# Kernel tuning notes

Hardware: AMD Instinct MI355X
Metric: run time of the kernel (lower is better)

Reference implementation:

```python
import jax, jax.numpy as jnp
import numpy as np

B, N, K1, M, D = 8, 4096, 17, 2, 256
NT = B * N          # total nodes
EPS = 1e-5          # PyG LayerNorm default eps


def setup_inputs() -> dict:
    key = jax.random.key(0)
    ks = jax.random.split(key, 13)
    s = 1.0 / np.sqrt(D)
    return {
        "x": jax.random.normal(ks[0], (NT, M, D), jnp.float32),
        "knn_edges": jax.random.randint(ks[1], (B, N, K1), 0, N),
        "edge_mask": jax.random.bernoulli(ks[2], 0.9, (B, N, K1)),
        "W0": jax.random.normal(ks[3], (D, D), jnp.float32) * s,
        "b0": jnp.zeros((D,), jnp.float32),
        "g0": jnp.ones((D,), jnp.float32),
        "be0": jnp.zeros((D,), jnp.float32),
        "a0": jnp.full((1,), 0.25, jnp.float32),
        "W1": jax.random.normal(ks[4], (D, D), jnp.float32) * s,
        "b1": jnp.zeros((D,), jnp.float32),
        "g1": jnp.ones((D,), jnp.float32),
        "be1": jnp.zeros((D,), jnp.float32),
        "a1": jnp.full((1,), 0.25, jnp.float32),
    }


def knn_to_edges(knn_edges, edge_mask):
    # drop self column 0, add per-graph batch offsets; keep fixed E with 0/1 weights
    e = knn_edges[:, :, 1:]                       # [B, N, K]
    m = edge_mask[:, :, 1:]
    off = (jnp.arange(B) * N)[:, None, None]      # [B,1,1]
    src = jnp.broadcast_to(jnp.arange(N)[None, :, None] + off, e.shape).reshape(-1)
    dst = (e + off).reshape(-1)
    w = m.reshape(-1).astype(jnp.float32)         # invalid edges -> weight 0
    return src, dst, w


def gcn_conv(h_in, W, b, src, dst, w):
    # PyG GCNConv: add self-loops (weight 1), symmetric normalization
    h = h_in @ W                                            # [NT, D]
    deg = jax.ops.segment_sum(w, dst, num_segments=NT) + 1.0
    dinv = jax.lax.rsqrt(deg)                               # [NT]
    norm = dinv[src] * w * dinv[dst]                        # [E]
    agg = jax.ops.segment_sum(norm[:, None] * h[src], dst, num_segments=NT)
    agg = agg + (dinv * dinv)[:, None] * h                  # self-loop term
    return agg + b


def graph_layernorm(x, g, b):
    # PyG LayerNorm mode='graph', batch=None: normalize over all nodes+features
    xc = x - jnp.mean(x)
    std = jnp.sqrt(jnp.mean(xc * xc))
    return g * (xc / (std + EPS)) + b


def prelu(x, a):
    return jnp.where(x >= 0, x, a * x)


def reference(x, knn_edges, edge_mask, W0, b0, g0, be0, a0, W1, b1, g1, be1, a1):
    src, dst, w = knn_to_edges(knn_edges, edge_mask)
    h = x[:, 0, :]                                          # [NT, D]
    for (W, b, g, be, a) in ((W0, b0, g0, be0, a0), (W1, b1, g1, be1, a1)):
        h = gcn_conv(h, W, b, src, dst, w)
        h = graph_layernorm(h, g, be)
        h = prelu(h, a)
    return h
```

## Files before the change

kernel.cpp:

```cpp
#include <hip/hip_runtime.h>
#include <hip/hip_bf16.h>
#include <stdint.h>

#define B_   8
#define N_   4096
#define K1_  17
#define D_   256
#define NT_  (B_*N_)
#define E16_ (NT_*16)
#define NP_  (NT_*D_)
#define EPS_ 1e-5f

typedef __attribute__((ext_vector_type(8))) short short8v;
typedef __attribute__((ext_vector_type(4))) short short4v;
typedef __attribute__((ext_vector_type(4))) float f32x4;

__device__ __forceinline__ unsigned short f2bfu(float f){
  unsigned u = __float_as_uint(f);
  unsigned r = (u + 0x7FFFu + ((u>>16)&1u)) >> 16;
  return (unsigned short)r;
}
__device__ __forceinline__ short f2bf(float f){ return (short)f2bfu(f); }
__device__ __forceinline__ unsigned pkbf(float lo, float hi){
  return (unsigned)f2bfu(lo) | ((unsigned)f2bfu(hi) << 16);
}
__device__ __forceinline__ float bf2f(short s){
  return __uint_as_float(((unsigned)(unsigned short)s) << 16);
}
__device__ __forceinline__ void unpack2(unsigned u, float& lo, float& hi){
  lo = __uint_as_float(u << 16);
  hi = __uint_as_float(u & 0xFFFF0000u);
}

__global__ __launch_bounds__(256) void k_prep(const float* __restrict__ W0,
                                              const float* __restrict__ W1,
                                              short* __restrict__ Wt0,
                                              short* __restrict__ Wt1,
                                              int* __restrict__ degcnt,
                                              const unsigned int* __restrict__ mw,
                                              int* __restrict__ flag){
  if (blockIdx.x < 128){
    const float* W  = (blockIdx.x & 1) ? W1  : W0;
    short*       Wt = (blockIdx.x & 1) ? Wt1 : Wt0;
    int tile = blockIdx.x >> 1;
    int ti = tile >> 3, tj = tile & 7;
    __shared__ float sm[32][33];
    int r = threadIdx.x >> 5, c = threadIdx.x & 31;
    #pragma unroll
    for (int i=0;i<4;i++)
      sm[r + i*8][c] = W[(ti*32 + r + i*8)*256 + tj*32 + c];
    __syncthreads();
    #pragma unroll
    for (int i=0;i<4;i++){
      int rr = r + i*8;
      Wt[(size_t)(tj*32 + rr)*256 + ti*32 + c] = f2bf(sm[c][rr]);
    }
  } else {
    int ib = blockIdx.x - 128;
    int i  = ib*256 + threadIdx.x;
    degcnt[i] = 0;
    if (ib == 0){
      __shared__ int s_int, s_f32;
      if (threadIdx.x==0){ s_int=1; s_f32=1; }
      __syncthreads();
      int bad_i=0, bad_f=0;
      #pragma unroll
      for (int j=0;j<4;j++){
        unsigned w = mw[threadIdx.x*4 + j];
        if (!(w==0u || w==1u))          bad_i=1;
        if (!(w==0u || w==0x3F800000u)) bad_f=1;
      }
      if (bad_i) atomicAnd(&s_int, 0);
      if (bad_f) atomicAnd(&s_f32, 0);
      __syncthreads();
      if (threadIdx.x==0) *flag = s_int ? 0 : (s_f32 ? 1 : 2);
    }
  }
}

__device__ __forceinline__ bool mask_at(const void* maskp, int f, int idx){
  if (f==0) return ((const int*)maskp)[idx] != 0;
  if (f==1) return ((const float*)maskp)[idx] != 0.0f;
  return ((const unsigned char*)maskp)[idx] != 0;
}

__global__ void k_deg(const int* __restrict__ knn, const void* __restrict__ maskp,
                      const int* __restrict__ flag, int* __restrict__ degcnt){
  int f = *flag;
  int e = blockIdx.x*blockDim.x + threadIdx.x;
  if (e >= E16_) return;
  int node = e >> 4;
  int k    = (e & 15) + 1;
  int idx  = node*K1_ + k;
  if (mask_at(maskp, f, idx)){
    int b   = node >> 12;
    int dst = knn[idx] + (b<<12);
    atomicAdd(&degcnt[dst], 1);
  }
}

__global__ void k_scan(const int* __restrict__ degcnt, int* __restrict__ rowptr,
                       int* __restrict__ fillptr, float* __restrict__ dinv){
  __shared__ int wsum[16];
  int t = threadIdx.x;
  int lane = t & 63, wid = t >> 6;
  int base = t*32;
  int loc[32]; int tot = 0;
  #pragma unroll
  for (int i=0;i<32;i++){ loc[i] = degcnt[base+i]; tot += loc[i]; }
  int inc = tot;
  #pragma unroll
  for (int off=1; off<64; off<<=1){
    int v = __shfl_up(inc, off, 64);
    if (lane >= off) inc += v;
  }
  if (lane == 63) wsum[wid] = inc;
  __syncthreads();
  int woff = 0;
  #pragma unroll
  for (int i=0;i<16;i++) if (i < wid) woff += wsum[i];
  int run = woff + inc - tot;
  #pragma unroll
  for (int i=0;i<32;i++){
    int v = base+i;
    rowptr[v]  = run;
    fillptr[v] = run;
    dinv[v]    = rsqrtf((float)loc[i] + 1.0f);
    run += loc[i];
  }
  if (t==1023) rowptr[NT_] = run;
}

__global__ __launch_bounds__(512, 4) void k_gemm_x_fill(const float* __restrict__ X,
                                                        const short* __restrict__ Wt,
                                                        short* __restrict__ C,
                                                        const int* __restrict__ knn,
                                                        const void* __restrict__ maskp,
                                                        const int* __restrict__ flag,
                                                        int* __restrict__ fillptr,
                                                        int* __restrict__ col){
  __shared__ short lds[2*128*64];
  if (blockIdx.x >= 512){
    int f = *flag;
    int e = (int)(blockIdx.x - 512)*512 + threadIdx.x;
    int node = e >> 4;
    int k    = (e & 15) + 1;
    int idx  = node*K1_ + k;
    if (mask_at(maskp, f, idx)){
      int b   = node >> 12;
      int dst = knn[idx] + (b<<12);
      int pos = atomicAdd(&fillptr[dst], 1);
      col[pos] = node;
    }
    return;
  }
  short* lA = lds;
  short* lB = lds + 128*64;
  int lb     = (int)(blockIdx.x & 7)*64 + (int)(blockIdx.x >> 3);
  int rowblk = lb >> 1, half = lb & 1;
  int rowB = rowblk*128, colB = half*128;

  int t    = threadIdx.x;
  int wave = t >> 6, lane = t & 63;
  int lr   = lane & 15, qg = lane >> 4;
  int wr   = wave >> 2, wc = wave & 3;

  f32x4 acc[4][2];
  #pragma unroll
  for (int m=0;m<4;m++)
    #pragma unroll
    for (int n=0;n<2;n++) acc[m][n] = (f32x4){0.f,0.f,0.f,0.f};

  int srow[2], sch[2];
  #pragma unroll
  for (int i=0;i<2;i++){ int e = t + i*512; srow[i] = e>>3; sch[i] = e&7; }

  float4 rax[2], ray[2]; uint4 rb[2];
  #pragma unroll
  for (int i=0;i<2;i++){
    const float* ap = X + (size_t)(rowB+srow[i])*512 + sch[i]*8;
    rax[i] = *(const float4*)ap;
    ray[i] = *(const float4*)(ap+4);
    rb[i]  = *(const uint4*)(Wt + (size_t)(colB+srow[i])*256 + sch[i]*8);
  }

  for (int kc=0; kc<4; kc++){
    if (kc) __syncthreads();
    #pragma unroll
    for (int i=0;i<2;i++){
      int ph = srow[i]*8 + (sch[i] ^ (srow[i]&7));
      uint4 cv;
      cv.x = pkbf(rax[i].x, rax[i].y); cv.y = pkbf(rax[i].z, rax[i].w);
      cv.z = pkbf(ray[i].x, ray[i].y); cv.w = pkbf(ray[i].z, ray[i].w);
      *(uint4*)(lA + ph*8) = cv;
      *(uint4*)(lB + ph*8) = rb[i];
    }
    __syncthreads();
    if (kc < 3){
      #pragma unroll
      for (int i=0;i<2;i++){
        const float* ap = X + (size_t)(rowB+srow[i])*512 + (kc+1)*64 + sch[i]*8;
        rax[i] = *(const float4*)ap;
        ray[i] = *(const float4*)(ap+4);
        rb[i]  = *(const uint4*)(Wt + (size_t)(colB+srow[i])*256 + (kc+1)*64 + sch[i]*8);
      }
    }
    #pragma unroll
    for (int ks=0; ks<2; ks++){
      short8v af[4], bfr[2];
      #pragma unroll
      for (int m=0;m<4;m++){
        int row = wr*64 + m*16 + lr;
        af[m] = *(const short8v*)(lA + (row*8 + ((ks*4+qg) ^ (row&7)))*8);
      }
      #pragma unroll
      for (int n=0;n<2;n++){
        int coln = wc*32 + n*16 + lr;
        bfr[n] = *(const short8v*)(lB + (coln*8 + ((ks*4+qg) ^ (coln&7)))*8);
      }
      #pragma unroll
      for (int m=0;m<4;m++)
        #pragma unroll
        for (int n=0;n<2;n++)
          acc[m][n] = __builtin_amdgcn_mfma_f32_16x16x32_bf16(af[m], bfr[n], acc[m][n], 0, 0, 0);
    }
  }

  __syncthreads();
  #pragma unroll
  for (int m=0;m<4;m++){
    int rloc = wr*64 + m*16 + qg*4;
    #pragma unroll
    for (int n=0;n<2;n++){
      int cloc = wc*32 + n*16 + lr;
      int cch  = cloc >> 3, cin = cloc & 7;
      #pragma unroll
      for (int r=0;r<4;r++){
        int row = rloc + r;
        lds[row*128 + ((cch ^ (row&7))<<3) + cin] = f2bf(acc[m][n][r]);
      }
    }
  }
  __syncthreads();
  #pragma unroll
  for (int i=0;i<4;i++){
    int e = t + i*512;
    int row = e >> 4, chunk = e & 15;
    uint4 v = *(const uint4*)(lds + row*128 + ((chunk ^ (row&7))<<3));
    *(uint4*)(C + (size_t)(rowB+row)*256 + colB + chunk*8) = v;
  }
}

__global__ __launch_bounds__(512, 4) void k_gemm_n(const unsigned* __restrict__ BaggU,
                                                   const float* __restrict__ g,
                                                   const float* __restrict__ be,
                                                   const float* __restrict__ aP,
                                                   const float* __restrict__ stats,
                                                   const short* __restrict__ Wt,
                                                   short* __restrict__ C){
  float mean = stats[0], inv = stats[1], a = aP[0];
  __shared__ short lds[2*128*64];
  short* lA = lds;
  short* lB = lds + 128*64;
  int lb     = (int)(blockIdx.x & 7)*64 + (int)(blockIdx.x >> 3);
  int rowblk = lb >> 1, half = lb & 1;
  int rowB = rowblk*128, colB = half*128;

  int t    = threadIdx.x;
  int wave = t >> 6, lane = t & 63;
  int lr   = lane & 15, qg = lane >> 4;
  int wr   = wave >> 2, wc = wave & 3;

  f32x4 acc[4][2];
  #pragma unroll
  for (int m=0;m<4;m++)
    #pragma unroll
    for (int n=0;n<2;n++) acc[m][n] = (f32x4){0.f,0.f,0.f,0.f};

  int srow[2], sch[2];
  #pragma unroll
  for (int i=0;i<2;i++){ int e = t + i*512; srow[i] = e>>3; sch[i] = e&7; }

  uint4 ra[2], rb[2];
  #pragma unroll
  for (int i=0;i<2;i++){
    ra[i] = *(const uint4*)(BaggU + (size_t)(rowB+srow[i])*128 + sch[i]*4);
    rb[i] = *(const uint4*)(Wt + (size_t)(colB+srow[i])*256 + sch[i]*8);
  }

  for (int kc=0; kc<4; kc++){
    if (kc) __syncthreads();
    #pragma unroll
    for (int i=0;i<2;i++){
      int ph = srow[i]*8 + (sch[i] ^ (srow[i]&7));
      int c0 = kc*64 + sch[i]*8;
      float4 g0 = *(const float4*)&g[c0],  g1 = *(const float4*)&g[c0+4];
      float4 e0 = *(const float4*)&be[c0], e1 = *(const float4*)&be[c0+4];
      float v[8];
      unpack2(ra[i].x, v[0], v[1]); unpack2(ra[i].y, v[2], v[3]);
      unpack2(ra[i].z, v[4], v[5]); unpack2(ra[i].w, v[6], v[7]);
      float gg[8] = {g0.x,g0.y,g0.z,g0.w,g1.x,g1.y,g1.z,g1.w};
      float eb[8] = {e0.x,e0.y,e0.z,e0.w,e1.x,e1.y,e1.z,e1.w};
      float o[8];
      #pragma unroll
      for (int j=0;j<8;j++){
        float tt = gg[j]*((v[j]-mean)*inv) + eb[j];
        o[j] = tt>=0.f ? tt : a*tt;
      }
      uint4 cv;
      cv.x = pkbf(o[0],o[1]); cv.y = pkbf(o[2],o[3]);
      cv.z = pkbf(o[4],o[5]); cv.w = pkbf(o[6],o[7]);
      *(uint4*)(lA + ph*8) = cv;
      *(uint4*)(lB + ph*8) = rb[i];
    }
    __syncthreads();
    if (kc < 3){
      #pragma unroll
      for (int i=0;i<2;i++){
        ra[i] = *(const uint4*)(BaggU + (size_t)(rowB+srow[i])*128 + (kc+1)*32 + sch[i]*4);
        rb[i] = *(const uint4*)(Wt + (size_t)(colB+srow[i])*256 + (kc+1)*64 + sch[i]*8);
      }
    }
    #pragma unroll
    for (int ks=0; ks<2; ks++){
      short8v af[4], bfr[2];
      #pragma unroll
      for (int m=0;m<4;m++){
        int row = wr*64 + m*16 + lr;
        af[m] = *(const short8v*)(lA + (row*8 + ((ks*4+qg) ^ (row&7)))*8);
      }
      #pragma unroll
      for (int n=0;n<2;n++){
        int coln = wc*32 + n*16 + lr;
        bfr[n] = *(const short8v*)(lB + (coln*8 + ((ks*4+qg) ^ (coln&7)))*8);
      }
      #pragma unroll
      for (int m=0;m<4;m++)
        #pragma unroll
        for (int n=0;n<2;n++)
          acc[m][n] = __builtin_amdgcn_mfma_f32_16x16x32_bf16(af[m], bfr[n], acc[m][n], 0, 0, 0);
    }
  }

  __syncthreads();
  #pragma unroll
  for (int m=0;m<4;m++){
    int rloc = wr*64 + m*16 + qg*4;
    #pragma unroll
    for (int n=0;n<2;n++){
      int cloc = wc*32 + n*16 + lr;
      int cch  = cloc >> 3, cin = cloc & 7;
      #pragma unroll
      for (int r=0;r<4;r++){
        int row = rloc + r;
        lds[row*128 + ((cch ^ (row&7))<<3) + cin] = f2bf(acc[m][n][r]);
      }
    }
  }
  __syncthreads();
  #pragma unroll
  for (int i=0;i<4;i++){
    int e = t + i*512;
    int row = e >> 4, chunk = e & 15;
    uint4 v = *(const uint4*)(lds + row*128 + ((chunk ^ (row&7))<<3));
    *(uint4*)(C + (size_t)(rowB+row)*256 + colB + chunk*8) = v;
  }
}

__global__ __launch_bounds__(256) void k_agg(const short* __restrict__ Ab,
    const int* __restrict__ rowptr, const int* __restrict__ col,
    const float* __restrict__ dinv, const float* __restrict__ bvec,
    unsigned* __restrict__ outU, float* __restrict__ partS, float* __restrict__ partQ){
  int bid  = (int)(blockIdx.x & 7) * 512 + (int)(blockIdx.x >> 3);
  int node = bid*8 + (threadIdx.x >> 5);
  int sub  = threadIdx.x & 31;
  int c0   = sub*8;
  float dv = dinv[node];

  float acc[8];
  {
    short8v s = *(const short8v*)&Ab[(size_t)node*256 + c0];
    #pragma unroll
    for (int i=0;i<8;i++) acc[i] = dv * bf2f(s[i]);
  }
  int j0 = rowptr[node], j1 = rowptr[node+1];
  for (int base=j0; base<j1; base+=32){
    int n = j1 - base; n = n < 32 ? n : 32;
    int   myc = (sub < n) ? col[base+sub] : 0;
    float myd = (sub < n) ? dinv[myc]     : 0.f;
    for (int j=0;j<n;j++){
      int   s  = __shfl(myc, j, 32);
      float ds = __shfl(myd, j, 32);
      short8v nb = *(const short8v*)&Ab[(size_t)s*256 + c0];
      #pragma unroll
      for (int i=0;i<8;i++) acc[i] += ds * bf2f(nb[i]);
    }
  }
  float sum=0.f, sq=0.f;
  float o[8];
  #pragma unroll
  for (int i=0;i<8;i++){
    float v = dv*acc[i] + bvec[c0+i];
    o[i] = v;
    sum += v; sq += v*v;
  }
  uint4 ov;
  ov.x = pkbf(o[0],o[1]); ov.y = pkbf(o[2],o[3]);
  ov.z = pkbf(o[4],o[5]); ov.w = pkbf(o[6],o[7]);
  *(uint4*)&outU[(size_t)node*128 + sub*4] = ov;

  #pragma unroll
  for (int off=16; off>0; off>>=1){
    sum += __shfl_down(sum, off, 32);
    sq  += __shfl_down(sq,  off, 32);
  }
  __shared__ float ls1[8], ls2[8];
  if (sub==0){ ls1[threadIdx.x>>5]=sum; ls2[threadIdx.x>>5]=sq; }
  __syncthreads();
  if (threadIdx.x==0){
    float a=0.f, b=0.f;
    #pragma unroll
    for (int i=0;i<8;i++){ a+=ls1[i]; b+=ls2[i]; }
    partS[bid]=a; partQ[bid]=b;
  }
}

__global__ void k_stats(const float* __restrict__ partS, const float* __restrict__ partQ,
                        float* __restrict__ stats){
  __shared__ double s1[1024], s2[1024];
  int t = threadIdx.x;
  double a=0.0, b=0.0;
  for (int i=t; i<4096; i+=1024){ a += (double)partS[i]; b += (double)partQ[i]; }
  s1[t]=a; s2[t]=b; __syncthreads();
  for (int off=512; off>0; off>>=1){
    if (t<off){ s1[t]+=s1[t+off]; s2[t]+=s2[t+off]; }
    __syncthreads();
  }
  if (t==0){
    double mean = s1[0] / (double)NP_;
    double var  = s2[0] / (double)NP_ - mean*mean;
    var = var > 0.0 ? var : 0.0;
    stats[0] = (float)mean;
    stats[1] = (float)(1.0 / (sqrt(var) + (double)EPS_));
  }
}

__global__ __launch_bounds__(256) void k_norm_f32(const unsigned* __restrict__ inU,
    const float* __restrict__ g, const float* __restrict__ be,
    const float* __restrict__ aP, const float* __restrict__ stats,
    float* __restrict__ out){
  float mean = stats[0], inv = stats[1], a = aP[0];
  int gid   = blockIdx.x*256 + threadIdx.x;
  int base8 = gid*8;
  int c0    = base8 & (D_-1);
  uint4 vin = *(const uint4*)&inU[gid*4];
  float4 g0 = *(const float4*)&g[c0],  g1 = *(const float4*)&g[c0+4];
  float4 e0 = *(const float4*)&be[c0], e1 = *(const float4*)&be[c0+4];
  float v[8];
  unpack2(vin.x, v[0], v[1]); unpack2(vin.y, v[2], v[3]);
  unpack2(vin.z, v[4], v[5]); unpack2(vin.w, v[6], v[7]);
  float gg[8] = {g0.x,g0.y,g0.z,g0.w,g1.x,g1.y,g1.z,g1.w};
  float eb[8] = {e0.x,e0.y,e0.z,e0.w,e1.x,e1.y,e1.z,e1.w};
  f32x4 o0, o1;
  #pragma unroll
  for (int i=0;i<8;i++){
    float tt = gg[i]*((v[i]-mean)*inv) + eb[i];
    tt = tt>=0.f ? tt : a*tt;
    if (i<4) o0[i] = tt; else o1[i-4] = tt;
  }
  *(f32x4*)&out[base8]     = o0;
  *(f32x4*)&out[base8 + 4] = o1;
}


extern "C" void kernel_launch(void* const* d_in, const int* in_sizes, int n_in,
                              void* d_out, int out_size, void* d_ws, size_t ws_size,
                              hipStream_t stream){
  const float* x    = (const float*)d_in[0];
  const int*   knn  = (const int*)  d_in[1];
  const void*  mask =               d_in[2];
  const float* W0   = (const float*)d_in[3];
  const float* b0   = (const float*)d_in[4];
  const float* g0   = (const float*)d_in[5];
  const float* be0  = (const float*)d_in[6];
  const float* a0   = (const float*)d_in[7];
  const float* W1   = (const float*)d_in[8];
  const float* b1   = (const float*)d_in[9];
  const float* g1   = (const float*)d_in[10];
  const float* be1  = (const float*)d_in[11];
  const float* a1   = (const float*)d_in[12];
  float* out = (float*)d_out;

  char* w = (char*)d_ws;
  size_t off = 0;
  auto alloc = [&](size_t bytes)->void*{
    void* p = w + off; off = (off + bytes + 255) & ~(size_t)255; return p;
  };
  int*      degcnt  = (int*)     alloc(NT_*4);
  int*      rowptr  = (int*)     alloc((NT_+1)*4);
  int*      fillptr = (int*)     alloc(NT_*4);
  int*      col     = (int*)     alloc(E16_*4);
  float*    dinv    = (float*)   alloc(NT_*4);
  float*    partS   = (float*)   alloc(4096*4);
  float*    partQ   = (float*)   alloc(4096*4);
  float*    stats   = (float*)   alloc(4*4);
  int*      flag    = (int*)     alloc(4);
  short*    Ab      = (short*)   alloc((size_t)NP_*2);
  unsigned* Bagg    = (unsigned*)alloc((size_t)NP_*2);
  short*    Wt0     = (short*)   alloc(256*256*2);
  short*    Wt1     = (short*)   alloc(256*256*2);

  hipLaunchKernelGGL(k_prep,  dim3(256),      dim3(256), 0, stream, W0, W1, Wt0, Wt1,
                     degcnt, (const unsigned int*)mask, flag);
  hipLaunchKernelGGL(k_deg,   dim3(E16_/256), dim3(256), 0, stream, knn, mask, flag, degcnt);
  hipLaunchKernelGGL(k_scan,  dim3(1),        dim3(1024),0, stream, degcnt, rowptr, fillptr, dinv);

  hipLaunchKernelGGL(k_gemm_x_fill, dim3(1536), dim3(512), 0, stream, x, Wt0, Ab,
                     knn, mask, flag, fillptr, col);
  hipLaunchKernelGGL(k_agg,    dim3(NT_/8),   dim3(256), 0, stream, Ab, rowptr, col, dinv, b0, Bagg, partS, partQ);
  hipLaunchKernelGGL(k_stats,  dim3(1),       dim3(1024),0, stream, partS, partQ, stats);

  hipLaunchKernelGGL(k_gemm_n, dim3(512),     dim3(512), 0, stream, Bagg, g0, be0, a0, stats, Wt1, Ab);
  hipLaunchKernelGGL(k_agg,    dim3(NT_/8),   dim3(256), 0, stream, Ab, rowptr, col, dinv, b1, Bagg, partS, partQ);
  hipLaunchKernelGGL(k_stats,  dim3(1),       dim3(1024),0, stream, partS, partQ, stats);
  hipLaunchKernelGGL(k_norm_f32, dim3(NP_/2048), dim3(256), 0, stream, Bagg, g1, be1, a1, stats, out);
}
```

Before: 161.4 us.

## Fold stats reduction into consumer kernels and deepen GEMM global prefetch

Removes the two single-block k_stats launches. Each k_gemm_n and k_norm_f32 block now reduces the 4096 partial sums itself in double precision. Both GEMM kernels now prefetch two K-chunks ahead in registers instead of one, and k_norm_f32 uses 1024 blocks that each process four elements per thread. This saves two launches and a serial single-block step, at the cost of every block redundantly reading 32 KB of partials and spending time on an LDS reduction before its main work. It also raises register pressure in the GEMMs.

```diff
diff --git a/kernel.cpp b/kernel.cpp
--- a/kernel.cpp
+++ b/kernel.cpp
@@ -129,6 +129,131 @@
     run += loc[i];
   }
   if (t==1023) rowptr[NT_] = run;
+}
+
+__device__ __forceinline__ void gx_issue(const float* __restrict__ X,
+                                         const short* __restrict__ Wt,
+                                         int rowB, int colB,
+                                         const int (&srow)[2], const int (&sch)[2],
+                                         int kc, float4 (&rax)[2], float4 (&ray)[2],
+                                         uint4 (&rb)[2]){
+  #pragma unroll
+  for (int i=0;i<2;i++){
+    const float* ap = X + (size_t)(rowB+srow[i])*512 + kc*64 + sch[i]*8;
+    rax[i] = *(const float4*)ap;
+    ray[i] = *(const float4*)(ap+4);
+    rb[i]  = *(const uint4*)(Wt + (size_t)(colB+srow[i])*256 + kc*64 + sch[i]*8);
+  }
+}
+
+__device__ __forceinline__ void gx_write(short* lA, short* lB,
+                                         const int (&srow)[2], const int (&sch)[2],
+                                         const float4 (&rax)[2], const float4 (&ray)[2],
+                                         const uint4 (&rb)[2]){
+  #pragma unroll
+  for (int i=0;i<2;i++){
+    int ph = srow[i]*8 + (sch[i] ^ (srow[i]&7));
+    uint4 cv;
+    cv.x = pkbf(rax[i].x, rax[i].y); cv.y = pkbf(rax[i].z, rax[i].w);
+    cv.z = pkbf(ray[i].x, ray[i].y); cv.w = pkbf(ray[i].z, ray[i].w);
+    *(uint4*)(lA + ph*8) = cv;
+    *(uint4*)(lB + ph*8) = rb[i];
+  }
+}
+
+__device__ __forceinline__ void gn_issue(const unsigned* __restrict__ BaggU,
+                                         const short* __restrict__ Wt,
+                                         int rowB, int colB,
+                                         const int (&srow)[2], const int (&sch)[2],
+                                         int kc, uint4 (&ra)[2], uint4 (&rb)[2]){
+  #pragma unroll
+  for (int i=0;i<2;i++){
+    ra[i] = *(const uint4*)(BaggU + (size_t)(rowB+srow[i])*128 + kc*32 + sch[i]*4);
+    rb[i] = *(const uint4*)(Wt + (size_t)(colB+srow[i])*256 + kc*64 + sch[i]*8);
+  }
+}
+
+__device__ __forceinline__ void gn_write(short* lA, short* lB,
+                                         const float* __restrict__ g,
+                                         const float* __restrict__ be,
+                                         float mean, float inv, float a, int kc,
+                                         const int (&srow)[2], const int (&sch)[2],
+                                         const uint4 (&ra)[2], const uint4 (&rb)[2]){
+  #pragma unroll
+  for (int i=0;i<2;i++){
+    int ph = srow[i]*8 + (sch[i] ^ (srow[i]&7));
+    int c0 = kc*64 + sch[i]*8;
+    float4 g0 = *(const float4*)&g[c0],  g1 = *(const float4*)&g[c0+4];
+    float4 e0 = *(const float4*)&be[c0], e1 = *(const float4*)&be[c0+4];
+    float v[8];
+    unpack2(ra[i].x, v[0], v[1]); unpack2(ra[i].y, v[2], v[3]);
+    unpack2(ra[i].z, v[4], v[5]); unpack2(ra[i].w, v[6], v[7]);
+    float gg[8] = {g0.x,g0.y,g0.z,g0.w,g1.x,g1.y,g1.z,g1.w};
+    float eb[8] = {e0.x,e0.y,e0.z,e0.w,e1.x,e1.y,e1.z,e1.w};
+    float o[8];
+    #pragma unroll
+    for (int j=0;j<8;j++){
+      float tt = gg[j]*((v[j]-mean)*inv) + eb[j];
+      o[j] = tt>=0.f ? tt : a*tt;
+    }
+    uint4 cv;
+    cv.x = pkbf(o[0],o[1]); cv.y = pkbf(o[2],o[3]);
+    cv.z = pkbf(o[4],o[5]); cv.w = pkbf(o[6],o[7]);
+    *(uint4*)(lA + ph*8) = cv;
+    *(uint4*)(lB + ph*8) = rb[i];
+  }
+}
+
+__device__ __forceinline__ void g_mfma(const short* lA, const short* lB,
+                                       int wr, int wc, int lr, int qg,
+                                       f32x4 (&acc)[4][2]){
+  #pragma unroll
+  for (int ks=0; ks<2; ks++){
+    short8v af[4], bfr[2];
+    #pragma unroll
+    for (int m=0;m<4;m++){
+      int row = wr*64 + m*16 + lr;
+      af[m] = *(const short8v*)(lA + (row*8 + ((ks*4+qg) ^ (row&7)))*8);
+    }
+    #pragma unroll
+    for (int n=0;n<2;n++){
+      int coln = wc*32 + n*16 + lr;
+      bfr[n] = *(const short8v*)(lB + (coln*8 + ((ks*4+qg) ^ (coln&7)))*8);
+    }
+    #pragma unroll
+    for (int m=0;m<4;m++)
+      #pragma unroll
+      for (int n=0;n<2;n++)
+        acc[m][n] = __builtin_amdgcn_mfma_f32_16x16x32_bf16(af[m], bfr[n], acc[m][n], 0, 0, 0);
+  }
+}
+
+__device__ __forceinline__ void g_store(short* lds, short* __restrict__ C,
+                                        int rowB, int colB, int t,
+                                        int wr, int wc, int lr, int qg,
+                                        const f32x4 (&acc)[4][2]){
+  #pragma unroll
+  for (int m=0;m<4;m++){
+    int rloc = wr*64 + m*16 + qg*4;
+    #pragma unroll
+    for (int n=0;n<2;n++){
+      int cloc = wc*32 + n*16 + lr;
+      int cch  = cloc >> 3, cin = cloc & 7;
+      #pragma unroll
+      for (int r=0;r<4;r++){
+        int row = rloc + r;
+        lds[row*128 + ((cch ^ (row&7))<<3) + cin] = f2bf(acc[m][n][r]);
+      }
+    }
+  }
+  __syncthreads();
+  #pragma unroll
+  for (int i=0;i<4;i++){
+    int e = t + i*512;
+    int row = e >> 4, chunk = e & 15;
+    uint4 v = *(const uint4*)(lds + row*128 + ((chunk ^ (row&7))<<3));
+    *(uint4*)(C + (size_t)(rowB+row)*256 + colB + chunk*8) = v;
+  }
 }
 
 __global__ __launch_bounds__(512, 4) void k_gemm_x_fill(const float* __restrict__ X,
@@ -175,91 +300,68 @@
   #pragma unroll
   for (int i=0;i<2;i++){ int e = t + i*512; srow[i] = e>>3; sch[i] = e&7; }
 
-  float4 rax[2], ray[2]; uint4 rb[2];
-  #pragma unroll
-  for (int i=0;i<2;i++){
-    const float* ap = X + (size_t)(rowB+srow[i])*512 + sch[i]*8;
-    rax[i] = *(const float4*)ap;
-    ray[i] = *(const float4*)(ap+4);
-    rb[i]  = *(const uint4*)(Wt + (size_t)(colB+srow[i])*256 + sch[i]*8);
-  }
-
-  for (int kc=0; kc<4; kc++){
-    if (kc) __syncthreads();
-    #pragma unroll
-    for (int i=0;i<2;i++){
-      int ph = srow[i]*8 + (sch[i] ^ (srow[i]&7));
-      uint4 cv;
-      cv.x = pkbf(rax[i].x, rax[i].y); cv.y = pkbf(rax[i].z, rax[i].w);
-      cv.z = pkbf(ray[i].x, ray[i].y); cv.w = pkbf(ray[i].z, ray[i].w);
-      *(uint4*)(lA + ph*8) = cv;
-      *(uint4*)(lB + ph*8) = rb[i];
-    }
-    __syncthreads();
-    if (kc < 3){
-      #pragma unroll
-      for (int i=0;i<2;i++){
-        const float* ap = X + (size_t)(rowB+srow[i])*512 + (kc+1)*64 + sch[i]*8;
-        rax[i] = *(const float4*)ap;
-        ray[i] = *(const float4*)(ap+4);
-        rb[i]  = *(const uint4*)(Wt + (size_t)(colB+srow[i])*256 + (kc+1)*64 + sch[i]*8);
-      }
-    }
-    #pragma unroll
-    for (int ks=0; ks<2; ks++){
-      short8v af[4], bfr[2];
-      #pragma unroll
-      for (int m=0;m<4;m++){
-        int row = wr*64 + m*16 + lr;
-        af[m] = *(const short8v*)(lA + (row*8 + ((ks*4+qg) ^ (row&7)))*8);
-      }
-      #pragma unroll
-      for (int n=0;n<2;n++){
-        int coln = wc*32 + n*16 + lr;
-        bfr[n] = *(const short8v*)(lB + (coln*8 + ((ks*4+qg) ^ (coln&7)))*8);
-      }
-      #pragma unroll
-      for (int m=0;m<4;m++)
-        #pragma unroll
-        for (int n=0;n<2;n++)
-          acc[m][n] = __builtin_amdgcn_mfma_f32_16x16x32_bf16(af[m], bfr[n], acc[m][n], 0, 0, 0);
-    }
-  }
-
-  __syncthreads();
-  #pragma unroll
-  for (int m=0;m<4;m++){
-    int rloc = wr*64 + m*16 + qg*4;
-    #pragma unroll
-    for (int n=0;n<2;n++){
-      int cloc = wc*32 + n*16 + lr;
-      int cch  = cloc >> 3, cin = cloc & 7;
-      #pragma unroll
-      for (int r=0;r<4;r++){
-        int row = rloc + r;
-        lds[row*128 + ((cch ^ (row&7))<<3) + cin] = f2bf(acc[m][n][r]);
-      }
-    }
-  }
-  __syncthreads();
-  #pragma unroll
-  for (int i=0;i<4;i++){
-    int e = t + i*512;
-    int row = e >> 4, chunk = e & 15;
-    uint4 v = *(const uint4*)(lds + row*128 + ((chunk ^ (row&7))<<3));
-    *(uint4*)(C + (size_t)(rowB+row)*256 + colB + chunk*8) = v;
-  }
+  float4 rax0[2], ray0[2]; uint4 rb0[2];
+  float4 rax1[2], ray1[2]; uint4 rb1[2];
+  gx_issue(X, Wt, rowB, colB, srow, sch, 0, rax0, ray0, rb0);
+  gx_issue(X, Wt, rowB, colB, srow, sch, 1, rax1, ray1, rb1);
+
+  gx_write(lA, lB, srow, sch, rax0, ray0, rb0);
+  __syncthreads();
+  gx_issue(X, Wt, rowB, colB, srow, sch, 2, rax0, ray0, rb0);
+  g_mfma(lA, lB, wr, wc, lr, qg, acc);
+  __syncthreads();
+  gx_write(lA, lB, srow, sch, rax1, ray1, rb1);
+  __syncthreads();
+  gx_issue(X, Wt, rowB, colB, srow, sch, 3, rax1, ray1, rb1);
+  g_mfma(lA, lB, wr, wc, lr, qg, acc);
+  __syncthreads();
+  gx_write(lA, lB, srow, sch, rax0, ray0, rb0);
+  __syncthreads();
+  g_mfma(lA, lB, wr, wc, lr, qg, acc);
+  __syncthreads();
+  gx_write(lA, lB, srow, sch, rax1, ray1, rb1);
+  __syncthreads();
+  g_mfma(lA, lB, wr, wc, lr, qg, acc);
+
+  __syncthreads();
+  g_store(lds, C, rowB, colB, t, wr, wc, lr, qg, acc);
 }
 
 __global__ __launch_bounds__(512, 4) void k_gemm_n(const unsigned* __restrict__ BaggU,
                                                    const float* __restrict__ g,
                                                    const float* __restrict__ be,
                                                    const float* __restrict__ aP,
-                                                   const float* __restrict__ stats,
+                                                   const float* __restrict__ partS,
+                                                   const float* __restrict__ partQ,
                                                    const short* __restrict__ Wt,
                                                    short* __restrict__ C){
-  float mean = stats[0], inv = stats[1], a = aP[0];
   __shared__ short lds[2*128*64];
+  float mean, inv;
+  {
+    double* sS = (double*)lds;
+    double* sQ = (double*)(lds + 4096);
+    double a=0.0, b=0.0;
+    for (int i=threadIdx.x; i<4096; i+=512){ a += (double)partS[i]; b += (double)partQ[i]; }
+    sS[threadIdx.x]=a; sQ[threadIdx.x]=b;
+    __syncthreads();
+    for (int off=256; off>0; off>>=1){
+      if ((int)threadIdx.x < off){ sS[threadIdx.x]+=sS[threadIdx.x+off]; sQ[threadIdx.x]+=sQ[threadIdx.x+off]; }
+      __syncthreads();
+    }
+    if (threadIdx.x==0){
+      double m   = sS[0] / (double)NP_;
+      double var = sQ[0] / (double)NP_ - m*m;
+      var = var > 0.0 ? var : 0.0;
+      ((float*)lds)[0] = (float)m;
+      ((float*)lds)[1] = (float)(1.0 / (sqrt(var) + (double)EPS_));
+    }
+    __syncthreads();
+    mean = ((float*)lds)[0];
+    inv  = ((float*)lds)[1];
+    __syncthreads();
+  }
+  float a = aP[0];
+
   short* lA = lds;
   short* lB = lds + 128*64;
   int lb     = (int)(blockIdx.x & 7)*64 + (int)(blockIdx.x >> 3);
@@ -281,90 +383,30 @@
   #pragma unroll
   for (int i=0;i<2;i++){ int e = t + i*512; srow[i] = e>>3; sch[i] = e&7; }
 
-  uint4 ra[2], rb[2];
-  #pragma unroll
-  for (int i=0;i<2;i++){
-    ra[i] = *(const uint4*)(BaggU + (size_t)(rowB+srow[i])*128 + sch[i]*4);
-    rb[i] = *(const uint4*)(Wt + (size_t)(colB+srow[i])*256 + sch[i]*8);
-  }
-
-  for (int kc=0; kc<4; kc++){
-    if (kc) __syncthreads();
-    #pragma unroll
-    for (int i=0;i<2;i++){
-      int ph = srow[i]*8 + (sch[i] ^ (srow[i]&7));
-      int c0 = kc*64 + sch[i]*8;
-      float4 g0 = *(const float4*)&g[c0],  g1 = *(const float4*)&g[c0+4];
-      float4 e0 = *(const float4*)&be[c0], e1 = *(const float4*)&be[c0+4];
-      float v[8];
-      unpack2(ra[i].x, v[0], v[1]); unpack2(ra[i].y, v[2], v[3]);
-      unpack2(ra[i].z, v[4], v[5]); unpack2(ra[i].w, v[6], v[7]);
-      float gg[8] = {g0.x,g0.y,g0.z,g0.w,g1.x,g1.y,g1.z,g1.w};
-      float eb[8] = {e0.x,e0.y,e0.z,e0.w,e1.x,e1.y,e1.z,e1.w};
-      float o[8];
-      #pragma unroll
-      for (int j=0;j<8;j++){
-        float tt = gg[j]*((v[j]-mean)*inv) + eb[j];
-        o[j] = tt>=0.f ? tt : a*tt;
-      }
-      uint4 cv;
-      cv.x = pkbf(o[0],o[1]); cv.y = pkbf(o[2],o[3]);
-      cv.z = pkbf(o[4],o[5]); cv.w = pkbf(o[6],o[7]);
-      *(uint4*)(lA + ph*8) = cv;
-      *(uint4*)(lB + ph*8) = rb[i];
-    }
-    __syncthreads();
-    if (kc < 3){
-      #pragma unroll
-      for (int i=0;i<2;i++){
-        ra[i] = *(const uint4*)(BaggU + (size_t)(rowB+srow[i])*128 + (kc+1)*32 + sch[i]*4);
-        rb[i] = *(const uint4*)(Wt + (size_t)(colB+srow[i])*256 + (kc+1)*64 + sch[i]*8);
-      }
-    }
-    #pragma unroll
-    for (int ks=0; ks<2; ks++){
-      short8v af[4], bfr[2];
-      #pragma unroll
-      for (int m=0;m<4;m++){
-        int row = wr*64 + m*16 + lr;
-        af[m] = *(const short8v*)(lA + (row*8 + ((ks*4+qg) ^ (row&7)))*8);
-      }
-      #pragma unroll
-      for (int n=0;n<2;n++){
-        int coln = wc*32 + n*16 + lr;
-        bfr[n] = *(const short8v*)(lB + (coln*8 + ((ks*4+qg) ^ (coln&7)))*8);
-      }
-      #pragma unroll
-      for (int m=0;m<4;m++)
-        #pragma unroll
-        for (int n=0;n<2;n++)
-          acc[m][n] = __builtin_amdgcn_mfma_f32_16x16x32_bf16(af[m], bfr[n], acc[m][n], 0, 0, 0);
-    }
-  }
-
-  __syncthreads();
-  #pragma unroll
-  for (int m=0;m<4;m++){
-    int rloc = wr*64 + m*16 + qg*4;
-    #pragma unroll
-    for (int n=0;n<2;n++){
-      int cloc = wc*32 + n*16 + lr;
-      int cch  = cloc >> 3, cin = cloc & 7;
-      #pragma unroll
-      for (int r=0;r<4;r++){
-        int row = rloc + r;
-        lds[row*128 + ((cch ^ (row&7))<<3) + cin] = f2bf(acc[m][n][r]);
-      }
-    }
-  }
-  __syncthreads();
-  #pragma unroll
-  for (int i=0;i<4;i++){
-    int e = t + i*512;
-    int row = e >> 4, chunk = e & 15;
-    uint4 v = *(const uint4*)(lds + row*128 + ((chunk ^ (row&7))<<3));
-    *(uint4*)(C + (size_t)(rowB+row)*256 + colB + chunk*8) = v;
-  }
+  uint4 ra0[2], rb0[2], ra1[2], rb1[2];
+  gn_issue(BaggU, Wt, rowB, colB, srow, sch, 0, ra0, rb0);
+  gn_issue(BaggU, Wt, rowB, colB, srow, sch, 1, ra1, rb1);
+
+  gn_write(lA, lB, g, be, mean, inv, a, 0, srow, sch, ra0, rb0);
+  __syncthreads();
+  gn_issue(BaggU, Wt, rowB, colB, srow, sch, 2, ra0, rb0);
+  g_mfma(lA, lB, wr, wc, lr, qg, acc);
+  __syncthreads();
+  gn_write(lA, lB, g, be, mean, inv, a, 1, srow, sch, ra1, rb1);
+  __syncthreads();
+  gn_issue(BaggU, Wt, rowB, colB, srow, sch, 3, ra1, rb1);
+  g_mfma(lA, lB, wr, wc, lr, qg, acc);
+  __syncthreads();
+  gn_write(lA, lB, g, be, mean, inv, a, 2, srow, sch, ra0, rb0);
+  __syncthreads();
+  g_mfma(lA, lB, wr, wc, lr, qg, acc);
+  __syncthreads();
+  gn_write(lA, lB, g, be, mean, inv, a, 3, srow, sch, ra1, rb1);
+  __syncthreads();
+  g_mfma(lA, lB, wr, wc, lr, qg, acc);
+
+  __syncthreads();
+  g_store(lds, C, rowB, colB, t, wr, wc, lr, qg, acc);
 }
 
 __global__ __launch_bounds__(256) void k_agg(const short* __restrict__ Ab,
@@ -425,51 +467,54 @@
   }
 }
 
-__global__ void k_stats(const float* __restrict__ partS, const float* __restrict__ partQ,
-                        float* __restrict__ stats){
-  __shared__ double s1[1024], s2[1024];
-  int t = threadIdx.x;
-  double a=0.0, b=0.0;
-  for (int i=t; i<4096; i+=1024){ a += (double)partS[i]; b += (double)partQ[i]; }
-  s1[t]=a; s2[t]=b; __syncthreads();
-  for (int off=512; off>0; off>>=1){
-    if (t<off){ s1[t]+=s1[t+off]; s2[t]+=s2[t+off]; }
-    __syncthreads();
-  }
-  if (t==0){
-    double mean = s1[0] / (double)NP_;
-    double var  = s2[0] / (double)NP_ - mean*mean;
-    var = var > 0.0 ? var : 0.0;
-    stats[0] = (float)mean;
-    stats[1] = (float)(1.0 / (sqrt(var) + (double)EPS_));
-  }
-}
-
 __global__ __launch_bounds__(256) void k_norm_f32(const unsigned* __restrict__ inU,
     const float* __restrict__ g, const float* __restrict__ be,
-    const float* __restrict__ aP, const float* __restrict__ stats,
-    float* __restrict__ out){
-  float mean = stats[0], inv = stats[1], a = aP[0];
-  int gid   = blockIdx.x*256 + threadIdx.x;
-  int base8 = gid*8;
-  int c0    = base8 & (D_-1);
-  uint4 vin = *(const uint4*)&inU[gid*4];
-  float4 g0 = *(const float4*)&g[c0],  g1 = *(const float4*)&g[c0+4];
-  float4 e0 = *(const float4*)&be[c0], e1 = *(const float4*)&be[c0+4];
-  float v[8];
-  unpack2(vin.x, v[0], v[1]); unpack2(vin.y, v[2], v[3]);
-  unpack2(vin.z, v[4], v[5]); unpack2(vin.w, v[6], v[7]);
-  float gg[8] = {g0.x,g0.y,g0.z,g0.w,g1.x,g1.y,g1.z,g1.w};
-  float eb[8] = {e0.x,e0.y,e0.z,e0.w,e1.x,e1.y,e1.z,e1.w};
-  f32x4 o0, o1;
-  #pragma unroll
-  for (int i=0;i<8;i++){
-    float tt = gg[i]*((v[i]-mean)*inv) + eb[i];
-    tt = tt>=0.f ? tt : a*tt;
-    if (i<4) o0[i] = tt; else o1[i-4] = tt;
-  }
-  *(f32x4*)&out[base8]     = o0;
-  *(f32x4*)&out[base8 + 4] = o1;
+    const float* __restrict__ aP, const float* __restrict__ partS,
+    const float* __restrict__ partQ, float* __restrict__ out){
+  __shared__ double sS[256], sQ[256];
+  __shared__ float s_mean, s_inv;
+  {
+    double a=0.0, b=0.0;
+    for (int i=threadIdx.x; i<4096; i+=256){ a += (double)partS[i]; b += (double)partQ[i]; }
+    sS[threadIdx.x]=a; sQ[threadIdx.x]=b;
+    __syncthreads();
+    for (int off=128; off>0; off>>=1){
+      if ((int)threadIdx.x < off){ sS[threadIdx.x]+=sS[threadIdx.x+off]; sQ[threadIdx.x]+=sQ[threadIdx.x+off]; }
+      __syncthreads();
+    }
+    if (threadIdx.x==0){
+      double m   = sS[0] / (double)NP_;
+      double var = sQ[0] / (double)NP_ - m*m;
+      var = var > 0.0 ? var : 0.0;
+      s_mean = (float)m;
+      s_inv  = (float)(1.0 / (sqrt(var) + (double)EPS_));
+    }
+    __syncthreads();
+  }
+  float mean = s_mean, inv = s_inv, a = aP[0];
+  #pragma unroll
+  for (int it=0; it<4; it++){
+    int gid   = it*(1024*256) + blockIdx.x*256 + threadIdx.x;
+    int base8 = gid*8;
+    int c0    = base8 & (D_-1);
+    uint4 vin = *(const uint4*)&inU[gid*4];
+    float4 g0 = *(const float4*)&g[c0],  g1 = *(const float4*)&g[c0+4];
+    float4 e0 = *(const float4*)&be[c0], e1 = *(const float4*)&be[c0+4];
+    float v[8];
+    unpack2(vin.x, v[0], v[1]); unpack2(vin.y, v[2], v[3]);
+    unpack2(vin.z, v[4], v[5]); unpack2(vin.w, v[6], v[7]);
+    float gg[8] = {g0.x,g0.y,g0.z,g0.w,g1.x,g1.y,g1.z,g1.w};
+    float eb[8] = {e0.x,e0.y,e0.z,e0.w,e1.x,e1.y,e1.z,e1.w};
+    f32x4 o0, o1;
+    #pragma unroll
+    for (int i=0;i<8;i++){
+      float tt = gg[i]*((v[i]-mean)*inv) + eb[i];
+      tt = tt>=0.f ? tt : a*tt;
+      if (i<4) o0[i] = tt; else o1[i-4] = tt;
+    }
+    *(f32x4*)&out[base8]     = o0;
+    *(f32x4*)&out[base8 + 4] = o1;
+  }
 }
 
 
@@ -503,7 +548,6 @@
   float*    dinv    = (float*)   alloc(NT_*4);
   float*    partS   = (float*)   alloc(4096*4);
   float*    partQ   = (float*)   alloc(4096*4);
-  float*    stats   = (float*)   alloc(4*4);
   int*      flag    = (int*)     alloc(4);
   short*    Ab      = (short*)   alloc((size_t)NP_*2);
   unsigned* Bagg    = (unsigned*)alloc((size_t)NP_*2);
@@ -518,10 +562,10 @@
   hipLaunchKernelGGL(k_gemm_x_fill, dim3(1536), dim3(512), 0, stream, x, Wt0, Ab,
                      knn, mask, flag, fillptr, col);
   hipLaunchKernelGGL(k_agg,    dim3(NT_/8),   dim3(256), 0, stream, Ab, rowptr, col, dinv, b0, Bagg, partS, partQ);
-  hipLaunchKernelGGL(k_stats,  dim3(1),       dim3(1024),0, stream, partS, partQ, stats);
-
-  hipLaunchKernelGGL(k_gemm_n, dim3(512),     dim3(512), 0, stream, Bagg, g0, be0, a0, stats, Wt1, Ab);
+
+  hipLaunchKernelGGL(k_gemm_n, dim3(512),     dim3(512), 0, stream, Bagg, g0, be0, a0,
+                     partS, partQ, Wt1, Ab);
   hipLaunchKernelGGL(k_agg,    dim3(NT_/8),   dim3(256), 0, stream, Ab, rowptr, col, dinv, b1, Bagg, partS, partQ);
-  hipLaunchKernelGGL(k_stats,  dim3(1),       dim3(1024),0, stream, partS, partQ, stats);
-  hipLaunchKernelGGL(k_norm_f32, dim3(NP_/2048), dim3(256), 0, stream, Bagg, g1, be1, a1, stats, out);
-}
+  hipLaunchKernelGGL(k_norm_f32, dim3(1024),  dim3(256), 0, stream, Bagg, g1, be1, a1,
+                     partS, partQ, out);
+}
```

Result: no change. 163.7 us (+1.4%).
